# Kernel tuning notes

Measured on AMD Instinct MI355X. Metric: run time of the kernel, lower is better.

## Reference

```python
import jax, jax.numpy as jnp
import numpy as np

PAD = 3


def _positions():
    """Exactly mirrors FoveatedConv2d._generate_sampling_positions, in forward's
    feature order: 9 inner taps, 16 ring5 positions, 24 ring7 positions."""
    pos = []
    for i in range(-1, 2):
        for j in range(-1, 2):
            pos.append([(i, j)])
    ring5 = [(i, j) for i in range(-2, 3) for j in range(-2, 3) if abs(i) == 2 or abs(j) == 2]
    for (i, j) in ring5:
        if i == -2 and abs(j) <= 1:
            p = [(i + k, j) for k in range(5)]
        elif i == 2 and abs(j) <= 1:
            p = [(i - k, j) for k in range(5)]
        elif j == -2 and abs(i) <= 1:
            p = [(i, j + k) for k in range(5)]
        elif j == 2 and abs(i) <= 1:
            p = [(i, j - k) for k in range(5)]
        elif i == -2 and j == -2:
            p = [(i + k, j) for k in range(5)] + [(i, j + k) for k in range(1, 5)]
        elif i == -2 and j == 2:
            p = [(i + k, j) for k in range(5)] + [(i, j - k) for k in range(1, 5)]
        elif i == 2 and j == -2:
            p = [(i - k, j) for k in range(5)] + [(i, j + k) for k in range(1, 5)]
        else:
            p = [(i - k, j) for k in range(5)] + [(i, j - k) for k in range(1, 5)]
        pos.append(p)
    ring7 = [(i, j) for i in range(-3, 4) for j in range(-3, 4) if abs(i) == 3 or abs(j) == 3]
    for (i, j) in ring7:
        if i == -3 and abs(j) <= 2:
            p = [(i + k, j) for k in range(15)]
        elif i == 3 and abs(j) <= 2:
            p = [(i - k, j) for k in range(15)]
        elif j == -3 and abs(i) <= 2:
            p = [(i, j + k) for k in range(25)]
        elif j == 3 and abs(i) <= 2:
            p = [(i, j - k) for k in range(25)]
        elif i == -3 and j == -3:
            p = [(i + k, j) for k in range(15)] + [(i, j + k) for k in range(1, 25)]
        elif i == -3 and j == 3:
            p = [(i + k, j) for k in range(15)] + [(i, j - k) for k in range(1, 25)]
        elif i == 3 and j == -3:
            p = [(i - k, j) for k in range(15)] + [(i, j + k) for k in range(1, 25)]
        else:
            p = [(i - k, j) for k in range(15)] + [(i, j - k) for k in range(1, 25)]
        pos.append(p)
    return pos


POSITIONS = _positions()  # 49 lists of (di, dj) offsets


def _foveated_features(x):
    B, C, H, W = x.shape
    xp = jnp.pad(x, ((0, 0), (0, 0), (PAD, PAD), (PAD, PAD)), mode='reflect')
    Hp, Wp = H + 2 * PAD, W + 2 * PAD
    h = jnp.arange(H)
    w = jnp.arange(W)
    feats = []
    for offs in POSITIONS:
        di = np.asarray([o[0] for o in offs])  # (K,)
        dj = np.asarray([o[1] for o in offs])
        hi = jnp.clip(h[None, :] + PAD + di[:, None], 0, Hp - 1)  # (K, H)
        wi = jnp.clip(w[None, :] + PAD + dj[:, None], 0, Wp - 1)  # (K, W)
        # gather all K samples for this ring position at every pixel: (B, C, K, H, W)
        s = xp[:, :, hi[:, :, None], wi[:, None, :]]
        feats.append(s.mean(axis=2))  # aggregation='mean'
    # stack in feature order -> (B, C, 49, H, W) -> (B, C*49, H, W), matching
    # torch's permute(0,1,4,2,3).view(B, C*49, H, W)
    return jnp.stack(feats, axis=2).reshape(B, C * 49, H, W)


def setup_inputs() -> dict:
    key = jax.random.key(0)
    kx, kw, kb = jax.random.split(key, 3)
    B, C, H, W, O = 4, 16, 192, 192, 64
    x = jax.random.normal(kx, (B, C, H, W), dtype=jnp.float32)
    weight = jax.random.normal(kw, (O, C * 49), dtype=jnp.float32) * 0.02
    bias = jax.random.normal(kb, (O,), dtype=jnp.float32) * 0.02
    return {"x": x, "weight": weight, "bias": bias}


def reference(x, weight, bias):
    f = _foveated_features(x)  # (B, C*49, H, W)
    # 1x1 conv == per-pixel GEMM
    return jnp.einsum('bchw,oc->bohw', f, weight) + bias[None, :, None, None]
```

## Files before the change

kernel.cpp:

```cpp
#include <hip/hip_runtime.h>
#include <hip/hip_bf16.h>

typedef __attribute__((ext_vector_type(8))) short short8v;
typedef __attribute__((ext_vector_type(4))) float float4v;
typedef unsigned short ushort;
typedef unsigned int uint;

namespace {

constexpr int Hh = 192, Ww = 192, Cc = 16, Oo = 64, Bb = 4;
constexpr int TH = 4, TW = 32, NT = 128;
constexpr int HW = Hh * Ww;
constexpr int NPL = Bb * Cc;
constexpr int PVG_PLANE = 236 * 198;
constexpr int PHG_PLANE = 198 * 236;
constexpr size_t PLANE = (size_t)Bb * Oo * HW;
constexpr size_t PREFIX_FLOATS = (size_t)NPL * (PVG_PLANE + PHG_PLANE);
constexpr size_t WBF_FLOATS = 65536 / 2;
constexpr size_t NEED_FULL = (PREFIX_FLOATS + WBF_FLOATS + 2 * PLANE) * 4;
constexpr int NPREF_T = 2 * NPL * 198;
constexpr int NPREF_B = (NPREF_T + 63) / 64;
constexpr int NWPREP_B = 65536 / 64;

struct FD { int hasV; int vdj, vi0, vi1; int hasH; int hdi, hj0, hj1; float inv_n; };

constexpr FD FT[49] = {
    {1,-1,-1,-1, 0,0,0,0, 1.f}, {1, 0,-1,-1, 0,0,0,0, 1.f}, {1, 1,-1,-1, 0,0,0,0, 1.f},
    {1,-1, 0, 0, 0,0,0,0, 1.f}, {1, 0, 0, 0, 0,0,0,0, 1.f}, {1, 1, 0, 0, 0,0,0,0, 1.f},
    {1,-1, 1, 1, 0,0,0,0, 1.f}, {1, 0, 1, 1, 0,0,0,0, 1.f}, {1, 1, 1, 1, 0,0,0,0, 1.f},
    {1,-2,-2, 2, 1,-2,-1, 2, 1.f/9.f},
    {1,-1,-2, 2, 0,0,0,0, 0.2f},
    {1, 0,-2, 2, 0,0,0,0, 0.2f},
    {1, 1,-2, 2, 0,0,0,0, 0.2f},
    {1, 2,-2, 2, 1,-2,-2, 1, 1.f/9.f},
    {0,0,0,0, 1,-1,-2, 2, 0.2f},
    {0,0,0,0, 1,-1,-2, 2, 0.2f},
    {0,0,0,0, 1, 0,-2, 2, 0.2f},
    {0,0,0,0, 1, 0,-2, 2, 0.2f},
    {0,0,0,0, 1, 1,-2, 2, 0.2f},
    {0,0,0,0, 1, 1,-2, 2, 0.2f},
    {1,-2,-2, 2, 1, 2,-1, 2, 1.f/9.f},
    {1,-1,-2, 2, 0,0,0,0, 0.2f},
    {1, 0,-2, 2, 0,0,0,0, 0.2f},
    {1, 1,-2, 2, 0,0,0,0, 0.2f},
    {1, 2,-2, 2, 1, 2,-2, 1, 1.f/9.f},
    {1,-3,-3,11, 1,-3,-2,21, 1.f/39.f},
    {1,-2,-3,11, 0,0,0,0, 1.f/15.f},
    {1,-1,-3,11, 0,0,0,0, 1.f/15.f},
    {1, 0,-3,11, 0,0,0,0, 1.f/15.f},
    {1, 1,-3,11, 0,0,0,0, 1.f/15.f},
    {1, 2,-3,11, 0,0,0,0, 1.f/15.f},
    {1, 3,-3,11, 1,-3,-21, 2, 1.f/39.f},
    {0,0,0,0, 1,-2,-3,21, 0.04f},
    {0,0,0,0, 1,-2,-21,3, 0.04f},
    {0,0,0,0, 1,-1,-3,21, 0.04f},
    {0,0,0,0, 1,-1,-21,3, 0.04f},
    {0,0,0,0, 1, 0,-3,21, 0.04f},
    {0,0,0,0, 1, 0,-21,3, 0.04f},
    {0,0,0,0, 1, 1,-3,21, 0.04f},
    {0,0,0,0, 1, 1,-21,3, 0.04f},
    {0,0,0,0, 1, 2,-3,21, 0.04f},
    {0,0,0,0, 1, 2,-21,3, 0.04f},
    {1,-3,-11,3, 1, 3,-2,21, 1.f/39.f},
    {1,-2,-11,3, 0,0,0,0, 1.f/15.f},
    {1,-1,-11,3, 0,0,0,0, 1.f/15.f},
    {1, 0,-11,3, 0,0,0,0, 1.f/15.f},
    {1, 1,-11,3, 0,0,0,0, 1.f/15.f},
    {1, 2,-11,3, 0,0,0,0, 1.f/15.f},
    {1, 3,-11,3, 1, 3,-21,2, 1.f/39.f},
};

__device__ __forceinline__ int mapIdx(int u) {
    if (u < 0) { u = -u; if (u > 3) u = 3; }
    else if (u > 191) { u = 382 - u; if (u < 188) u = 188; }
    return u;
}

__device__ __forceinline__ ushort f2bf(float f) {
    __hip_bfloat16 h = __float2bfloat16(f);
    return __builtin_bit_cast(ushort, h);
}

__global__ __launch_bounds__(64)
void prep(const float* __restrict__ x, const float* __restrict__ wgt,
          float* __restrict__ pvg, float* __restrict__ phg, ushort* __restrict__ wbf)
{
    if (blockIdx.x >= NPREF_B) {
        const int t = (blockIdx.x - NPREF_B) * 64 + threadIdx.x;
        const int k = t & 63, o = (t >> 6) & 63, c = t >> 12;
        wbf[t] = (k < 49) ? f2bf(wgt[o * 784 + c * 49 + k]) : (ushort)0;
        return;
    }
    const int t = blockIdx.x * 64 + threadIdx.x;
    if (t >= NPREF_T) return;
    const bool isPV = t < NPL * 198;
    const int u = isPV ? t : t - NPL * 198;
    const int plane = u / 198;
    const int q     = u - plane * 198;
    const float* xp = x + (size_t)plane * HW;
    if (isPV) {
        const int wsrc = mapIdx(q - 3);
        float* pv = pvg + (size_t)plane * PVG_PLANE + q;
        float r = 0.f;
        pv[0] = 0.f;
        for (int t0 = 0; t0 < 235; t0 += 5) {
            float v0 = xp[mapIdx(t0 - 21) * Ww + wsrc];
            float v1 = xp[mapIdx(t0 - 20) * Ww + wsrc];
            float v2 = xp[mapIdx(t0 - 19) * Ww + wsrc];
            float v3 = xp[mapIdx(t0 - 18) * Ww + wsrc];
            float v4 = xp[mapIdx(t0 - 17) * Ww + wsrc];
            float* pd = pv + (size_t)(t0 + 1) * 198;
            r += v0; pd[0]   = r;
            r += v1; pd[198] = r;
            r += v2; pd[396] = r;
            r += v3; pd[594] = r;
            r += v4; pd[792] = r;
        }
    } else {
        const int rsrc = mapIdx(q - 3) * Ww;
        float* ph = phg + (size_t)plane * PHG_PLANE + (size_t)q * 236;
        float r = 0.f;
        ph[0] = 0.f;
        for (int t0 = 0; t0 < 235; t0 += 5) {
            float v0 = xp[rsrc + mapIdx(t0 - 21)];
            float v1 = xp[rsrc + mapIdx(t0 - 20)];
            float v2 = xp[rsrc + mapIdx(t0 - 19)];
            float v3 = xp[rsrc + mapIdx(t0 - 18)];
            float v4 = xp[rsrc + mapIdx(t0 - 17)];
            float* pd = ph + t0 + 1;
            r += v0; pd[0] = r;
            r += v1; pd[1] = r;
            r += v2; pd[2] = r;
            r += v3; pd[3] = r;
            r += v4; pd[4] = r;
        }
    }
}

template<int NC, bool DIRECT>
__global__ __launch_bounds__(NT, 3)
void fova22(const ushort* __restrict__ wbf, const float* __restrict__ bias,
            const float* __restrict__ pvg, const float* __restrict__ phg,
            float* __restrict__ dst)
{
    constexpr int HALVES = Cc / NC;
    __shared__ ushort featB[NT][66];
    __shared__ ushort wlds[64][72];
    __shared__ float  pvt[27][40];
    __shared__ float  pht[10][76];

    const int tid  = threadIdx.x;
    const int lane = tid & 63;
    const int wv   = tid >> 6;
    const int w0   = blockIdx.x * TW;
    const int h0   = blockIdx.y * TH;
    const int bz   = blockIdx.z;
    const int b    = (HALVES == 1) ? bz : (bz >> 1);
    const int half = (HALVES == 1) ? 0  : (bz & 1);
    const int c0   = half * NC;
    const int ph_  = tid >> 5;
    const int pw   = tid & 31;

    float4v acc[4][4];
#pragma unroll
    for (int i = 0; i < 4; ++i)
#pragma unroll
        for (int j = 0; j < 4; ++j) acc[i][j] = (float4v)(0.f);

#pragma unroll
    for (int f = 49; f < 64; ++f) featB[tid][f] = 0;

    const float* pvsrc = pvg + (size_t)(b * Cc + c0) * PVG_PLANE + (size_t)(h0 + 10) * 198 + w0;
    const float* phsrc = phg + (size_t)(b * Cc + c0) * PHG_PLANE + (size_t)h0 * 236 + w0;
    const ushort* wsrc0 = wbf + (c0 << 12) + tid * 32;

    for (int idx = tid; idx < 27 * 38; idx += NT) {
        int r = idx / 38, c = idx - r * 38;
        pvt[r][c] = pvsrc[r * 198 + c];
    }
    for (int idx = tid; idx < 10 * 75; idx += NT) {
        int r = idx / 75, c = idx - r * 75;
        pht[r][c] = phsrc[r * 236 + c];
    }
    __syncthreads();

    for (int cc = 0; cc < NC; ++cc) {
        short8v wreg[4];
#pragma unroll
        for (int q = 0; q < 4; ++q)
            wreg[q] = *(const short8v*)(&wsrc0[q * 8]);

        {
            auto FV = [&](int f) -> float {
                float s = 0.f;
                if (FT[f].hasV)
                    s += pvt[ph_ + FT[f].vi1 + 12][pw + 3 + FT[f].vdj]
                       - pvt[ph_ + FT[f].vi0 + 11][pw + 3 + FT[f].vdj];
                if (FT[f].hasH)
                    s += pht[ph_ + 3 + FT[f].hdi][pw + 21 + FT[f].hj1 + 1]
                       - pht[ph_ + 3 + FT[f].hdi][pw + 21 + FT[f].hj0];
                return s * FT[f].inv_n;
            };
            uint* fb32 = reinterpret_cast<uint*>(&featB[tid][0]);
#pragma unroll
            for (int j = 0; j < 24; ++j)
                fb32[j] = (uint)f2bf(FV(2 * j)) | ((uint)f2bf(FV(2 * j + 1)) << 16);
            featB[tid][48] = f2bf(FV(48));
        }
        {
            const int base = tid * 4;
#pragma unroll
            for (int q = 0; q < 4; ++q) {
                const int idx = base + q;
                *(short8v*)(&wlds[idx >> 3][(idx & 7) * 8]) = wreg[q];
            }
        }
        __syncthreads();

        float pvr[9], phr[6];
        const bool more = (cc + 1 < NC);
        if (more) {
            const float* pvn = pvsrc + PVG_PLANE;
            const float* phn = phsrc + PHG_PLANE;
#pragma unroll
            for (int k = 0; k < 9; ++k) {
                int idx = tid + k * NT;
                if (idx < 27 * 38) pvr[k] = pvn[(idx / 38) * 198 + (idx % 38)];
            }
#pragma unroll
            for (int k = 0; k < 6; ++k) {
                int idx = tid + k * NT;
                if (idx < 10 * 75) phr[k] = phn[(idx / 75) * 236 + (idx % 75)];
            }
        }

        {
            const int olo = lane & 15, kg = lane >> 4;
#pragma unroll
            for (int kc = 0; kc < 2; ++kc) {
                const int k0 = kc * 32 + kg * 8;
                short8v afr[4];
#pragma unroll
                for (int ob = 0; ob < 4; ++ob) {
                    const int o = ob * 16 + olo;
                    afr[ob] = *(const short8v*)(&wlds[o][k0]);
                }
                short8v bfr[4];
#pragma unroll
                for (int nb = 0; nb < 4; ++nb) {
                    const int p = wv * 64 + nb * 16 + olo;
                    const uint* bp = (const uint*)(&featB[p][k0]);
                    uint4 u;
                    u.x = bp[0]; u.y = bp[1]; u.z = bp[2]; u.w = bp[3];
                    bfr[nb] = __builtin_bit_cast(short8v, u);
                }
#pragma unroll
                for (int ob = 0; ob < 4; ++ob)
#pragma unroll
                    for (int nb = 0; nb < 4; ++nb)
                        acc[ob][nb] = __builtin_amdgcn_mfma_f32_16x16x32_bf16(
                            afr[ob], bfr[nb], acc[ob][nb], 0, 0, 0);
            }
        }

        if (more) {
#pragma unroll
            for (int k = 0; k < 9; ++k) {
                int idx = tid + k * NT;
                if (idx < 27 * 38) pvt[idx / 38][idx % 38] = pvr[k];
            }
#pragma unroll
            for (int k = 0; k < 6; ++k) {
                int idx = tid + k * NT;
                if (idx < 10 * 75) pht[idx / 75][idx % 75] = phr[k];
            }
        }
        __syncthreads();

        pvsrc += PVG_PLANE; phsrc += PHG_PLANE; wsrc0 += 4096;
    }

    float* dbase = DIRECT ? dst : (dst + (size_t)half * PLANE);
#pragma unroll
    for (int ob = 0; ob < 4; ++ob)
#pragma unroll
        for (int nb = 0; nb < 4; ++nb) {
            const int p = wv * 64 + nb * 16 + (lane & 15);
            const int hh = h0 + (p >> 5), ww2 = w0 + (p & 31);
            const int o0 = ob * 16 + ((lane >> 4) << 2);
            float4v a = acc[ob][nb];
#pragma unroll
            for (int r = 0; r < 4; ++r) {
                const int o = o0 + r;
                float v = DIRECT ? (a[r] + bias[o]) : a[r];
                dbase[(((size_t)b * Oo + o) * Hh + hh) * Ww + ww2] = v;
            }
        }
}

__global__ __launch_bounds__(256)
void reduce2(const float4* __restrict__ p, const float* __restrict__ bias,
             float4* __restrict__ out)
{
    const int n4 = (int)(PLANE / 4);
    for (int i = blockIdx.x * 256 + threadIdx.x; i < n4; i += gridDim.x * 256) {
        float4 a = p[i];
        float4 b = p[i + n4];
        const int o = (i / 9216) & 63;
        const float bo = bias[o];
        float4 r;
        r.x = a.x + b.x + bo; r.y = a.y + b.y + bo;
        r.z = a.z + b.z + bo; r.w = a.w + b.w + bo;
        out[i] = r;
    }
}

}

extern "C" void kernel_launch(void* const* d_in, const int* in_sizes, int n_in,
                              void* d_out, int out_size, void* d_ws, size_t ws_size,
                              hipStream_t stream) {
    (void)in_sizes; (void)n_in; (void)out_size;
    const float* x    = (const float*)d_in[0];
    const float* wgt  = (const float*)d_in[1];
    const float* bias = (const float*)d_in[2];
    float* out        = (float*)d_out;

    float* pvg  = (float*)d_ws;
    float* phg  = pvg + (size_t)NPL * PVG_PLANE;
    ushort* wbf = (ushort*)(phg + (size_t)NPL * PHG_PLANE);

    prep<<<dim3(NPREF_B + NWPREP_B), dim3(64), 0, stream>>>(x, wgt, pvg, phg, wbf);

    dim3 block(NT);
    if (ws_size >= NEED_FULL) {
        float* part = (float*)d_ws + PREFIX_FLOATS + WBF_FLOATS;
        dim3 grid(Ww / TW, Hh / TH, Bb * 2);
        fova22<8, false><<<grid, block, 0, stream>>>(wbf, bias, pvg, phg, part);
        reduce2<<<dim3(2048), dim3(256), 0, stream>>>((const float4*)part, bias, (float4*)out);
    } else {
        dim3 grid(Ww / TW, Hh / TH, Bb);
        fova22<16, true><<<grid, block, 0, stream>>>(wbf, bias, pvg, phg, out);
    }
}
```

Baseline: 113.0 us.

## Parallelize horizontal prefix scan with wave shuffles and read it directly from global

The horizontal prefix-sum pass in prep is now computed with one wavefront per row using a shuffle-based inclusive scan, instead of one thread serially walking 235 elements. This fixes the poorly coalesced, latency-bound serial loop. The main kernel no longer stages the horizontal prefix tile in LDS. Each thread instead reads its horizontal prefix values straight from global memory (L1/L2), which removes the LDS tile, its prefetch registers and its stores, at the cost of scattered global loads inside the feature loop. Prep block size also grows from 64 to 256 threads.

Measured after the change: 144.8 us. 28.1% more time.

```diff
diff --git a/kernel.cpp b/kernel.cpp
--- a/kernel.cpp
+++ b/kernel.cpp
@@ -18,9 +18,11 @@
 constexpr size_t PREFIX_FLOATS = (size_t)NPL * (PVG_PLANE + PHG_PLANE);
 constexpr size_t WBF_FLOATS = 65536 / 2;
 constexpr size_t NEED_FULL = (PREFIX_FLOATS + WBF_FLOATS + 2 * PLANE) * 4;
-constexpr int NPREF_T = 2 * NPL * 198;
-constexpr int NPREF_B = (NPREF_T + 63) / 64;
-constexpr int NWPREP_B = 65536 / 64;
+constexpr int PH_ROWS  = NPL * 198;
+constexpr int PH_B     = PH_ROWS / 4;
+constexpr int PV_B     = (NPL * 198 + 255) / 256;
+constexpr int WP_B     = 65536 / 256;
+constexpr int PREP_B   = PH_B + PV_B + WP_B;
 
 struct FD { int hasV; int vdj, vi0, vi1; int hasH; int hdi, hj0, hj1; float inv_n; };
 
@@ -81,24 +83,41 @@
     return __builtin_bit_cast(ushort, h);
 }
 
-__global__ __launch_bounds__(64)
+__global__ __launch_bounds__(256)
 void prep(const float* __restrict__ x, const float* __restrict__ wgt,
           float* __restrict__ pvg, float* __restrict__ phg, ushort* __restrict__ wbf)
 {
-    if (blockIdx.x >= NPREF_B) {
-        const int t = (blockIdx.x - NPREF_B) * 64 + threadIdx.x;
-        const int k = t & 63, o = (t >> 6) & 63, c = t >> 12;
-        wbf[t] = (k < 49) ? f2bf(wgt[o * 784 + c * 49 + k]) : (ushort)0;
+    const int bid = blockIdx.x, tid = threadIdx.x;
+    if (bid < PH_B) {
+        const int lane = tid & 63;
+        const int row  = bid * 4 + (tid >> 6);
+        const int plane = row / 198;
+        const int q     = row - plane * 198;
+        const float* xp = x + (size_t)plane * HW;
+        const int rsrc  = mapIdx(q - 3) * Ww;
+        float* ph = phg + (size_t)plane * PHG_PLANE + (size_t)q * 236;
+        if (lane == 0) ph[0] = 0.f;
+        float carry = 0.f;
+#pragma unroll
+        for (int ck = 0; ck < 4; ++ck) {
+            const int idx = ck * 64 + lane;
+            float v = (idx < 235) ? xp[rsrc + mapIdx(idx - 21)] : 0.f;
+#pragma unroll
+            for (int d = 1; d < 64; d <<= 1) {
+                float t2 = __shfl_up(v, d);
+                if (lane >= d) v += t2;
+            }
+            if (idx < 235) ph[idx + 1] = v + carry;
+            carry += __shfl(v, 63);
+        }
         return;
     }
-    const int t = blockIdx.x * 64 + threadIdx.x;
-    if (t >= NPREF_T) return;
-    const bool isPV = t < NPL * 198;
-    const int u = isPV ? t : t - NPL * 198;
-    const int plane = u / 198;
-    const int q     = u - plane * 198;
-    const float* xp = x + (size_t)plane * HW;
-    if (isPV) {
+    if (bid < PH_B + PV_B) {
+        const int t = (bid - PH_B) * 256 + tid;
+        if (t >= NPL * 198) return;
+        const int plane = t / 198;
+        const int q     = t - plane * 198;
+        const float* xp = x + (size_t)plane * HW;
         const int wsrc = mapIdx(q - 3);
         float* pv = pvg + (size_t)plane * PVG_PLANE + q;
         float r = 0.f;
@@ -116,30 +135,18 @@
             r += v3; pd[594] = r;
             r += v4; pd[792] = r;
         }
-    } else {
-        const int rsrc = mapIdx(q - 3) * Ww;
-        float* ph = phg + (size_t)plane * PHG_PLANE + (size_t)q * 236;
-        float r = 0.f;
-        ph[0] = 0.f;
-        for (int t0 = 0; t0 < 235; t0 += 5) {
-            float v0 = xp[rsrc + mapIdx(t0 - 21)];
-            float v1 = xp[rsrc + mapIdx(t0 - 20)];
-            float v2 = xp[rsrc + mapIdx(t0 - 19)];
-            float v3 = xp[rsrc + mapIdx(t0 - 18)];
-            float v4 = xp[rsrc + mapIdx(t0 - 17)];
-            float* pd = ph + t0 + 1;
-            r += v0; pd[0] = r;
-            r += v1; pd[1] = r;
-            r += v2; pd[2] = r;
-            r += v3; pd[3] = r;
-            r += v4; pd[4] = r;
-        }
+        return;
+    }
+    {
+        const int t = (bid - PH_B - PV_B) * 256 + tid;
+        const int k = t & 63, o = (t >> 6) & 63, c = t >> 12;
+        wbf[t] = (k < 49) ? f2bf(wgt[o * 784 + c * 49 + k]) : (ushort)0;
     }
 }
 
 template<int NC, bool DIRECT>
 __global__ __launch_bounds__(NT, 3)
-void fova22(const ushort* __restrict__ wbf, const float* __restrict__ bias,
+void fova23(const ushort* __restrict__ wbf, const float* __restrict__ bias,
             const float* __restrict__ pvg, const float* __restrict__ phg,
             float* __restrict__ dst)
 {
@@ -147,7 +154,6 @@
     __shared__ ushort featB[NT][66];
     __shared__ ushort wlds[64][72];
     __shared__ float  pvt[27][40];
-    __shared__ float  pht[10][76];
 
     const int tid  = threadIdx.x;
     const int lane = tid & 63;
@@ -160,6 +166,7 @@
     const int c0   = half * NC;
     const int ph_  = tid >> 5;
     const int pw   = tid & 31;
+    const int h    = h0 + ph_, w = w0 + pw;
 
     float4v acc[4][4];
 #pragma unroll
@@ -171,16 +178,12 @@
     for (int f = 49; f < 64; ++f) featB[tid][f] = 0;
 
     const float* pvsrc = pvg + (size_t)(b * Cc + c0) * PVG_PLANE + (size_t)(h0 + 10) * 198 + w0;
-    const float* phsrc = phg + (size_t)(b * Cc + c0) * PHG_PLANE + (size_t)h0 * 236 + w0;
+    const float* phb   = phg + (size_t)(b * Cc + c0) * PHG_PLANE + (size_t)(h + 3) * 236 + (w + 21);
     const ushort* wsrc0 = wbf + (c0 << 12) + tid * 32;
 
     for (int idx = tid; idx < 27 * 38; idx += NT) {
         int r = idx / 38, c = idx - r * 38;
         pvt[r][c] = pvsrc[r * 198 + c];
-    }
-    for (int idx = tid; idx < 10 * 75; idx += NT) {
-        int r = idx / 75, c = idx - r * 75;
-        pht[r][c] = phsrc[r * 236 + c];
     }
     __syncthreads();
 
@@ -197,8 +200,7 @@
                     s += pvt[ph_ + FT[f].vi1 + 12][pw + 3 + FT[f].vdj]
                        - pvt[ph_ + FT[f].vi0 + 11][pw + 3 + FT[f].vdj];
                 if (FT[f].hasH)
-                    s += pht[ph_ + 3 + FT[f].hdi][pw + 21 + FT[f].hj1 + 1]
-                       - pht[ph_ + 3 + FT[f].hdi][pw + 21 + FT[f].hj0];
+                    s += phb[FT[f].hdi * 236 + (FT[f].hj1 + 1)] - phb[FT[f].hdi * 236 + FT[f].hj0];
                 return s * FT[f].inv_n;
             };
             uint* fb32 = reinterpret_cast<uint*>(&featB[tid][0]);
@@ -217,20 +219,14 @@
         }
         __syncthreads();
 
-        float pvr[9], phr[6];
+        float pvr[9];
         const bool more = (cc + 1 < NC);
         if (more) {
             const float* pvn = pvsrc + PVG_PLANE;
-            const float* phn = phsrc + PHG_PLANE;
 #pragma unroll
             for (int k = 0; k < 9; ++k) {
                 int idx = tid + k * NT;
                 if (idx < 27 * 38) pvr[k] = pvn[(idx / 38) * 198 + (idx % 38)];
-            }
-#pragma unroll
-            for (int k = 0; k < 6; ++k) {
-                int idx = tid + k * NT;
-                if (idx < 10 * 75) phr[k] = phn[(idx / 75) * 236 + (idx % 75)];
             }
         }
 
@@ -269,15 +265,10 @@
                 int idx = tid + k * NT;
                 if (idx < 27 * 38) pvt[idx / 38][idx % 38] = pvr[k];
             }
-#pragma unroll
-            for (int k = 0; k < 6; ++k) {
-                int idx = tid + k * NT;
-                if (idx < 10 * 75) pht[idx / 75][idx % 75] = phr[k];
-            }
         }
         __syncthreads();
 
-        pvsrc += PVG_PLANE; phsrc += PHG_PLANE; wsrc0 += 4096;
+        pvsrc += PVG_PLANE; phb += PHG_PLANE; wsrc0 += 4096;
     }
 
     float* dbase = DIRECT ? dst : (dst + (size_t)half * PLANE);
@@ -330,16 +321,16 @@
     float* phg  = pvg + (size_t)NPL * PVG_PLANE;
     ushort* wbf = (ushort*)(phg + (size_t)NPL * PHG_PLANE);
 
-    prep<<<dim3(NPREF_B + NWPREP_B), dim3(64), 0, stream>>>(x, wgt, pvg, phg, wbf);
+    prep<<<dim3(PREP_B), dim3(256), 0, stream>>>(x, wgt, pvg, phg, wbf);
 
     dim3 block(NT);
     if (ws_size >= NEED_FULL) {
         float* part = (float*)d_ws + PREFIX_FLOATS + WBF_FLOATS;
         dim3 grid(Ww / TW, Hh / TH, Bb * 2);
-        fova22<8, false><<<grid, block, 0, stream>>>(wbf, bias, pvg, phg, part);
+        fova23<8, false><<<grid, block, 0, stream>>>(wbf, bias, pvg, phg, part);
         reduce2<<<dim3(2048), dim3(256), 0, stream>>>((const float4*)part, bias, (float4*)out);
     } else {
         dim3 grid(Ww / TW, Hh / TH, Bb);
-        fova22<16, true><<<grid, block, 0, stream>>>(wbf, bias, pvg, phg, out);
-    }
-}
+        fova23<16, true><<<grid, block, 0, stream>>>(wbf, bias, pvg, phg, out);
+    }
+}
```
